# Optimization experiments

Measured on AMD Instinct MI355X. Metric: run time of the kernel, lower is better.

The kernel has to match this reference:

```python
import jax, jax.numpy as jnp
import numpy as np

IMG_H, IMG_W = 240, 320
NEAR, FAR = 0.1, 10.0
CHUNK = 64  # triangles rasterized per scan step
CAM_K = np.array([[286.2057, 0.0, 162.6306],
                  [0.0, 286.7852, 121.0245],
                  [0.0, 0.0, 1.0]], np.float32)


def build_projection(cam, w, h, x0=0, y0=0, nc=NEAR, fc=FAR):
    q = -(fc + nc) / float(fc - nc)
    qn = -2.0 * fc * nc / float(fc - nc)
    proj = np.array([
        [2 * cam[0, 0] / w, -2 * cam[0, 1] / w, (-2 * cam[0, 2] + w + 2 * x0) / w, 0],
        [0, -2 * cam[1, 1] / h, (-2 * cam[1, 2] + h + 2 * y0) / h, 0],
        [0, 0, q, qn],
        [0, 0, -1, 0]], dtype=np.float64)
    proj[1, :] *= -1.0
    return jnp.asarray(proj.T, jnp.float32)


def vertex_normals(verts, faces):
    # per-face normal scattered to its vertices then renormalized
    # (equals dirt lighting.vertex_normals_pre_split on split meshes)
    v0, v1, v2 = verts[faces[:, 0]], verts[faces[:, 1]], verts[faces[:, 2]]
    fn = jnp.cross(v1 - v0, v2 - v0)
    fn = fn / jnp.maximum(jnp.linalg.norm(fn, axis=1, keepdims=True), 1e-12)
    vn = (jnp.zeros_like(verts)
          .at[faces[:, 0]].add(fn)
          .at[faces[:, 1]].add(fn)
          .at[faces[:, 2]].add(fn))
    return vn / jnp.maximum(jnp.linalg.norm(vn, axis=1, keepdims=True), 1e-12)


def transform_vertices(vertices, pose, faces, proj):
    vert_obj = jnp.concatenate([vertices, jnp.ones_like(vertices[:, -1:])], axis=1)  # [V,4]
    normals = vertex_normals(vert_obj[:, :3], faces)
    gl = jnp.array([[1., 0., 0.], [0., -1., 0.], [0., 0., -1.]], jnp.float32)
    rot = gl @ pose[:3, :3]
    # replicate the flat-list surgery: cam_pose[:3,:3]=gl@R, negate t_y, t_z
    cam_pose = pose.at[:3, :3].set(rot).at[1, 3].multiply(-1.0).at[2, 3].multiply(-1.0)
    view = cam_pose.T
    vert_cam = vert_obj @ view                                   # [V,4]
    vert_3d = vert_obj[:, :3] @ pose[:3, :3].T + pose[:3, 3]     # [V,3]
    vert_clip = vert_cam @ proj                                  # [V,4]
    return vert_obj, vert_3d, vert_clip, normals


def rasterise(vert_clip, colors, faces, H, W):
    # z-buffered triangle rasterization with perspective-correct barycentric
    # interpolation, processed in chunks of CHUNK triangles via lax.scan.
    eps = 1e-9
    wc = vert_clip[:, 3]
    inv_w = 1.0 / jnp.where(jnp.abs(wc) > eps, wc, eps)
    ndc = vert_clip[:, :3] * inv_w[:, None]
    px = (ndc[:, 0] + 1.0) * 0.5 * W   # screen x
    py = (1.0 - ndc[:, 1]) * 0.5 * H   # screen y (row 0 at top)
    pz = ndc[:, 2]

    tpx, tpy, tpz = px[faces], py[faces], pz[faces]   # [F,3]
    tiw = inv_w[faces]                                # [F,3]
    tcol = colors[faces]                              # [F,3,C]
    tval = jnp.all(wc[faces] > 1e-6, axis=1)          # all verts in front

    F = faces.shape[0]
    pad = (-F) % CHUNK
    def padf(a):
        if pad == 0:
            return a
        return jnp.concatenate([a, jnp.zeros((pad,) + a.shape[1:], a.dtype)], 0)
    tpx, tpy, tpz, tiw, tcol = padf(tpx), padf(tpy), padf(tpz), padf(tiw), padf(tcol)
    tval = padf(tval)
    n_steps = (F + pad) // CHUNK
    resh = lambda a: a.reshape((n_steps, CHUNK) + a.shape[1:])
    xs = tuple(map(resh, (tpx, tpy, tpz, tiw, tcol, tval)))

    Xg = (jnp.arange(W, dtype=jnp.float32) + 0.5)[None, :, None]  # pixel centers
    Yg = (jnp.arange(H, dtype=jnp.float32) + 0.5)[:, None, None]
    BIG = jnp.float32(1e9)

    def step(carry, chunk):
        zbuf, cbuf = carry
        cpx, cpy, cpz, ciw, ccol, cval = chunk
        ax, ay = cpx[:, 0], cpy[:, 0]
        bx, by = cpx[:, 1], cpy[:, 1]
        cx, cy = cpx[:, 2], cpy[:, 2]
        area = (bx - ax) * (cy - ay) - (by - ay) * (cx - ax)            # [Fc]
        inv_area = 1.0 / jnp.where(jnp.abs(area) > 1e-12, area, 1e-12)
        # normalized edge functions (barycentrics), [H,W,Fc]
        e0 = ((Xg - bx) * (cy - by) - (Yg - by) * (cx - bx)) * inv_area
        e1 = ((Xg - cx) * (ay - cy) - (Yg - cy) * (ax - cx)) * inv_area
        e2 = 1.0 - e0 - e1
        depth = e0 * cpz[:, 0] + e1 * cpz[:, 1] + e2 * cpz[:, 2]        # screen-linear z
        inside = ((e0 >= 0) & (e1 >= 0) & (e2 >= 0) & cval
                  & (jnp.abs(area) > 1e-12) & (depth >= -1.0) & (depth <= 1.0))
        dmask = jnp.where(inside, depth, BIG)
        best = jnp.argmin(dmask, axis=2)                                # [H,W]
        bidx = best[..., None]
        bdepth = jnp.take_along_axis(dmask, bidx, 2)[..., 0]
        take = bdepth < zbuf
        b0 = jnp.take_along_axis(e0, bidx, 2)[..., 0]
        b1 = jnp.take_along_axis(e1, bidx, 2)[..., 0]
        b2 = 1.0 - b0 - b1
        piw = jnp.stack([b0, b1, b2], -1) * ciw[best]                   # [H,W,3]
        den = jnp.sum(piw, -1, keepdims=True)
        den = jnp.where(jnp.abs(den) > 1e-12, den, 1e-12)
        col = jnp.einsum('hwk,hwkc->hwc', piw / den, ccol[best])        # persp-correct
        zbuf = jnp.where(take, bdepth, zbuf)
        cbuf = jnp.where(take[..., None], col, cbuf)
        return (zbuf, cbuf), None

    zbuf0 = jnp.full((H, W), BIG, jnp.float32)
    cbuf0 = jnp.zeros((H, W, colors.shape[1]), jnp.float32)
    (_, cbuf), _ = jax.lax.scan(jax.checkpoint(step), (zbuf0, cbuf0), xs)
    return cbuf


def setup_inputs() -> dict:
    key = jax.random.key(0)
    k1, k2 = jax.random.split(key)
    V, F = 12288, 4096
    vertices = 0.15 * jax.random.normal(k1, (1, V, 3), jnp.float32)
    faces = jax.random.randint(k2, (1, F, 3), 0, V, jnp.int32)
    pose = jnp.eye(4, dtype=jnp.float32).at[2, 3].set(0.6)  # object 0.6m in front
    return {"vertices": vertices, "faces": faces, "poses": pose[None]}


def reference(vertices, faces, poses):
    proj = build_projection(CAM_K, IMG_W, IMG_H)
    faces0 = jnp.asarray(faces[0], jnp.int32)
    vert_obj, vert_3d, vert_clip, normals = transform_vertices(vertices[0], poses[0], faces0, proj)
    colors = jnp.concatenate(
        [jnp.ones_like(vert_obj[:, :1]), vert_3d, normals, vert_obj], axis=1)  # [V,11]
    g = rasterise(vert_clip, colors, faces0, IMG_H, IMG_W)  # [H,W,11]
    return g[None]
```

## Files before the change

### kernel.cpp

```cpp
#include <hip/hip_runtime.h>
#include <math.h>

#pragma clang fp contract(off)

#define IMG_H 240
#define IMG_W 320
#define NPX   (IMG_H * IMG_W)
#define NCH   11
#define NCHP  12
#define NSLICE 8
#define CULL_M 1e-3f
#define EZ_M   1e-5f
#define NBIN   256

struct ProjM { float m[16]; };

__device__ __forceinline__ int zbin(float zm) {
  float t = fminf(fmaxf((zm + 1.0f) * 128.0f, 0.0f), 255.0f);
  int b = (int)t;
  if ((float)b * 0.0078125f - 1.0f > zm) b = (b > 0) ? b - 1 : 0;
  return b;
}

extern "C" __global__ void k_init(float* __restrict__ vnacc, int n3v,
                                  unsigned long long* __restrict__ zkey,
                                  int* __restrict__ hist) {
  int i = blockIdx.x * 256 + threadIdx.x;
  if (i < n3v) vnacc[i] = 0.0f;
  if (i < NPX) zkey[i] = ~0ull;
  if (i < NBIN) hist[i] = 0;
}

__device__ __forceinline__ void xform(float x, float y, float z,
                                      const float* __restrict__ pose,
                                      const ProjM& P,
                                      float& px, float& py, float& pz,
                                      float& iw, float& wc) {
  float c0 = ((x*pose[0]     + y*pose[1])     + z*pose[2])     + pose[3];
  float c1 = ((x*(-pose[4])  + y*(-pose[5]))  + z*(-pose[6]))  + (-pose[7]);
  float c2 = ((x*(-pose[8])  + y*(-pose[9]))  + z*(-pose[10])) + (-pose[11]);
  float c3 = ((x*pose[12]    + y*pose[13])    + z*pose[14])    + pose[15];
  float q0 = ((c0*P.m[0]  + c1*P.m[1])  + c2*P.m[2])  + c3*P.m[3];
  float q1 = ((c0*P.m[4]  + c1*P.m[5])  + c2*P.m[6])  + c3*P.m[7];
  float q2 = ((c0*P.m[8]  + c1*P.m[9])  + c2*P.m[10]) + c3*P.m[11];
  float q3 = ((c0*P.m[12] + c1*P.m[13]) + c2*P.m[14]) + c3*P.m[15];
  wc = q3;
  float denw = (fabsf(wc) > 1e-9f) ? wc : 1e-9f;
  iw = 1.0f / denw;
  float ndx = q0 * iw, ndy = q1 * iw;
  pz = q2 * iw;
  px = ((ndx + 1.0f) * 0.5f) * (float)IMG_W;
  py = ((1.0f - ndy) * 0.5f) * (float)IMG_H;
}

extern "C" __global__ void k_face(const float* __restrict__ verts,
                                  const int* __restrict__ faces,
                                  const float* __restrict__ pose,
                                  ProjM P,
                                  float* __restrict__ vnacc,
                                  float4* __restrict__ frec,
                                  float4* __restrict__ fbb,
                                  float4* __restrict__ fe,
                                  int4*  __restrict__ fidx,
                                  float* __restrict__ fzmin,
                                  int*   __restrict__ hist, int F) {
  int f = blockIdx.x * 64 + threadIdx.x;
  if (f >= F) return;
  int i0 = faces[3*f+0], i1 = faces[3*f+1], i2 = faces[3*f+2];
  float x0 = verts[3*i0+0], y0 = verts[3*i0+1], z0 = verts[3*i0+2];
  float x1 = verts[3*i1+0], y1 = verts[3*i1+1], z1 = verts[3*i1+2];
  float x2 = verts[3*i2+0], y2 = verts[3*i2+1], z2 = verts[3*i2+2];

  {
    float ux = x1 - x0, uy = y1 - y0, uz = z1 - z0;
    float vx = x2 - x0, vy = y2 - y0, vz = z2 - z0;
    float fx = uy*vz - uz*vy;
    float fy = uz*vx - ux*vz;
    float fz = ux*vy - uy*vx;
    float n = sqrtf((fx*fx + fy*fy) + fz*fz);
    float d = fmaxf(n, 1e-12f);
    fx = fx / d; fy = fy / d; fz = fz / d;
    atomicAdd(&vnacc[3*i0+0], fx); atomicAdd(&vnacc[3*i0+1], fy); atomicAdd(&vnacc[3*i0+2], fz);
    atomicAdd(&vnacc[3*i1+0], fx); atomicAdd(&vnacc[3*i1+1], fy); atomicAdd(&vnacc[3*i1+2], fz);
    atomicAdd(&vnacc[3*i2+0], fx); atomicAdd(&vnacc[3*i2+1], fy); atomicAdd(&vnacc[3*i2+2], fz);
  }

  float ax, ay, pz0, iw0, w0;  xform(x0, y0, z0, pose, P, ax, ay, pz0, iw0, w0);
  float bx, by, pz1, iw1, w1;  xform(x1, y1, z1, pose, P, bx, by, pz1, iw1, w1);
  float cx, cy, pz2, iw2, w2;  xform(x2, y2, z2, pose, P, cx, cy, pz2, iw2, w2);

  float area = (bx - ax) * (cy - ay) - (by - ay) * (cx - ax);
  float inva = 1.0f / ((fabsf(area) > 1e-12f) ? area : 1e-12f);
  bool valid = (w0 > 1e-6f) && (w1 > 1e-6f) && (w2 > 1e-6f) && (fabsf(area) > 1e-12f);
  float rax = 2.0f*cx - ax, ray = 2.0f*cy - ay;
  float rbx = 2.0f*cx - bx, rby = 2.0f*cy - by;
  float minx = fminf(cx, fminf(rax, rbx)), maxx = fmaxf(cx, fmaxf(rax, rbx));
  float miny = fminf(cy, fminf(ray, rby)), maxy = fmaxf(cy, fmaxf(ray, rby));
  frec[4*f+0] = make_float4(bx, by, cy - by, cx - bx);
  frec[4*f+1] = make_float4(cx, cy, ay - cy, ax - cx);
  frec[4*f+2] = make_float4(inva, pz0, pz1, pz2);
  frec[4*f+3] = make_float4(iw0, iw1, iw2, 0.0f);
  fbb[f] = valid ? make_float4(minx, maxx, miny, maxy)
                 : make_float4(1e30f, -1e30f, 1e30f, -1e30f);
  fidx[f] = make_int4(i0, i1, i2, 0);

  float zm = valid ? fminf(pz0, fminf(pz1, pz2)) : __builtin_huge_valf();
  fzmin[f] = zm;
  atomicAdd(&hist[zbin(zm)], 1);

  {
    double dbx = bx, dby = by, dcx = cx, dcy = cy, dax = ax, day = ay;
    double dinv = (double)inva;
    double d0 = dcy - dby, d1 = dcx - dbx;
    double d2 = day - dcy, d3 = dax - dcx;
    double a0 = d0 * dinv, b0 = -d1 * dinv, c0 = (dby * d1 - dbx * d0) * dinv;
    double a1 = d2 * dinv, b1 = -d3 * dinv, c1 = (dcy * d3 - dcx * d2) * dinv;
    fe[2*f+0] = make_float4((float)a0, (float)b0, (float)c0, 0.0f);
    fe[2*f+1] = make_float4((float)a1, (float)b1, (float)c1, 0.0f);
  }
}

extern "C" __global__ void k_scan(const int* __restrict__ hist,
                                  int* __restrict__ binoff) {
  __shared__ int s[NBIN];
  int t = threadIdx.x;
  int v = hist[t];
  s[t] = v;
  __syncthreads();
  for (int o = 1; o < NBIN; o <<= 1) {
    int x = (t >= o) ? s[t - o] : 0;
    __syncthreads();
    s[t] += x;
    __syncthreads();
  }
  binoff[t] = s[t] - v;
}

extern "C" __global__ void k_scatter(const float* __restrict__ fzmin,
                                     int* __restrict__ binoff,
                                     const float4* __restrict__ fbb,
                                     const float4* __restrict__ fe,
                                     int*   __restrict__ forig,
                                     float* __restrict__ szmin,
                                     float* __restrict__ smon,
                                     float4* __restrict__ fbbs,
                                     float4* __restrict__ fes, int F) {
  int f = blockIdx.x * 256 + threadIdx.x;
  if (f >= F) return;
  float zm = fzmin[f];
  int b = zbin(zm);
  int pos = atomicAdd(&binoff[b], 1);
  forig[pos] = f;
  szmin[pos] = zm;
  smon[pos]  = (float)b * 0.0078125f - 1.0f;
  fbbs[pos]  = fbb[f];
  fes[2*pos+0] = fe[2*f+0];
  fes[2*pos+1] = fe[2*f+1];
}

extern "C" __global__ void k_vertex(const float* __restrict__ verts,
                                    const float* __restrict__ vnacc,
                                    const float* __restrict__ pose,
                                    float4* __restrict__ colors, int V) {
  int i = blockIdx.x * 64 + threadIdx.x;
  if (i >= V) return;
  float x = verts[3*i+0], y = verts[3*i+1], z = verts[3*i+2];

  float nx = vnacc[3*i+0], ny = vnacc[3*i+1], nz = vnacc[3*i+2];
  float nn = sqrtf((nx*nx + ny*ny) + nz*nz);
  float nm = fmaxf(nn, 1e-12f);
  nx = nx / nm; ny = ny / nm; nz = nz / nm;

  float v3x = ((x*pose[0] + y*pose[1]) + z*pose[2])  + pose[3];
  float v3y = ((x*pose[4] + y*pose[5]) + z*pose[6])  + pose[7];
  float v3z = ((x*pose[8] + y*pose[9]) + z*pose[10]) + pose[11];

  colors[3*i+0] = make_float4(1.0f, v3x, v3y, v3z);
  colors[3*i+1] = make_float4(nx, ny, nz, x);
  colors[3*i+2] = make_float4(y, z, 1.0f, 0.0f);
}

extern "C" __global__ __launch_bounds__(256)
void k_rasterA(const float4* __restrict__ frec,
               const float4* __restrict__ fbbs,
               const float4* __restrict__ fes,
               const int*    __restrict__ forig,
               const float*  __restrict__ szmin,
               const float*  __restrict__ smon,
               unsigned long long* __restrict__ zkey,
               int F) {
  int t = threadIdx.x;
  int wave = t >> 6;
  int lane = t & 63;
  int sx = (wave & 1) * 8, sy = (wave >> 1) * 8;
  int pxi = blockIdx.x * 16 + sx + (lane & 7);
  int pyi = blockIdx.y * 16 + sy + (lane >> 3);
  float X = (float)pxi + 0.5f;
  float Y = (float)pyi + 0.5f;
  float tXlo = (float)(blockIdx.x * 16 + sx) + 0.5f, tXhi = tXlo + 7.0f;
  float tYlo = (float)(blockIdx.y * 16 + sy) + 0.5f, tYhi = tYlo + 7.0f;
  size_t pix = (size_t)pyi * IMG_W + pxi;

  float bestd = 1.0f + 1.0e-3f;
  int   besti = -1;

  int nchunk = (F + 63) >> 6;
  for (int c = blockIdx.z; c < nchunk; c += NSLICE) {
    int base = c << 6;

    float pb = bestd;
    {
      unsigned long long k = __hip_atomic_load(&zkey[pix], __ATOMIC_RELAXED,
                                               __HIP_MEMORY_SCOPE_AGENT);
      if (k != ~0ull) {
        unsigned int ub = (unsigned int)(k >> 32);
        unsigned int fb = (ub & 0x80000000u) ? (ub & 0x7FFFFFFFu) : ~ub;
        pb = fminf(pb, __uint_as_float(fb));
      }
    }
    float pbm = pb;
    #pragma unroll
    for (int o = 32; o > 0; o >>= 1) pbm = fmaxf(pbm, __shfl_xor(pbm, o));

    if (pbm <= smon[base] - EZ_M) break;

    int i = base + lane;
    bool ov = false;
    if (i < F && szmin[i] < pbm + EZ_M) {
      float4 bb = fbbs[i];
      ov = (bb.x - 1.0f <= tXhi) && (bb.y + 1.0f >= tXlo) &&
           (bb.z - 1.0f <= tYhi) && (bb.w + 1.0f >= tYlo);
      if (ov) {
        float4 E0 = fes[2*i+0];
        float4 E1 = fes[2*i+1];
        float pa0 = E0.x * tXlo, pb0 = E0.x * tXhi;
        float qa0 = E0.y * tYlo, qb0 = E0.y * tYhi;
        float e0mx = (fmaxf(pa0, pb0) + fmaxf(qa0, qb0)) + E0.z;
        float pa1 = E1.x * tXlo, pb1 = E1.x * tXhi;
        float qa1 = E1.y * tYlo, qb1 = E1.y * tYhi;
        float e1mx = (fmaxf(pa1, pb1) + fmaxf(qa1, qb1)) + E1.z;
        float e0mn = (fminf(pa0, pb0) + fminf(qa0, qb0)) + E0.z;
        float e1mn = (fminf(pa1, pb1) + fminf(qa1, qb1)) + E1.z;
        float e2mx = (1.0f - e0mn) - e1mn;
        ov = (e0mx >= -CULL_M) && (e1mx >= -CULL_M) && (e2mx >= -CULL_M);
      }
    }
    unsigned long long mask = __ballot(ov);
    bool improved = false;

    while (mask) {
      int j = __builtin_ctzll(mask);
      mask &= mask - 1;
      int ju = __builtin_amdgcn_readfirstlane(forig[base + j]);
      const float4* fr = frec + (size_t)ju * 4;
      float4 A = fr[0];
      float4 B = fr[1];
      float4 C = fr[2];
      float t0 = (X - A.x) * A.z;
      float t1 = (Y - A.y) * A.w;
      float e0 = (t0 - t1) * C.x;
      float t2 = (X - B.x) * B.z;
      float t3 = (Y - B.y) * B.w;
      float e1 = (t2 - t3) * C.x;
      float e2 = (1.0f - e0) - e1;
      float depth = ((e0 * C.y) + (e1 * C.z)) + (e2 * C.w);
      bool inside = (e0 >= 0.0f) && (e1 >= 0.0f) && (e2 >= 0.0f) &&
                    (depth >= -1.0f) && (depth <= 1.0f);
      if (inside && depth < bestd) {
        bestd = depth; besti = ju; improved = true;
      }
    }

    if (improved && bestd <= pb) {
      unsigned int ub = __float_as_uint(bestd);
      ub = (ub & 0x80000000u) ? ~ub : (ub | 0x80000000u);
      unsigned long long key = ((unsigned long long)ub << 32) | (unsigned int)besti;
      atomicMin(&zkey[pix], key);
    }
  }
}

extern "C" __global__ __launch_bounds__(256)
void k_resolve(const unsigned long long* __restrict__ zkey,
               const float4* __restrict__ frec,
               const float4* __restrict__ colors,
               const int4* __restrict__ fidx,
               float* __restrict__ out) {
  __shared__ float sOut[256 * NCH];
  int t = threadIdx.x;
  int p = blockIdx.x * 256 + t;
  int pyi = p / IMG_W, pxi = p - pyi * IMG_W;
  float X = (float)pxi + 0.5f;
  float Y = (float)pyi + 0.5f;
  unsigned long long key = zkey[p];

  float oc[NCH];
  if (key != ~0ull) {
    int besti = (int)(key & 0xFFFFFFFFu);
    const float4* fr = frec + (size_t)besti * 4;
    float4 A = fr[0], B = fr[1], C = fr[2], D = fr[3];
    float t0 = (X - A.x) * A.z;
    float t1 = (Y - A.y) * A.w;
    float e0 = (t0 - t1) * C.x;
    float t2 = (X - B.x) * B.z;
    float t3 = (Y - B.y) * B.w;
    float e1 = (t2 - t3) * C.x;
    float b2 = (1.0f - e0) - e1;
    float p0 = e0 * D.x, p1 = e1 * D.y, p2 = b2 * D.z;
    float den = (p0 + p1) + p2;
    if (!(fabsf(den) > 1e-12f)) den = 1e-12f;
    float u0 = p0 / den, u1 = p1 / den, u2 = p2 / den;
    int4 vi = fidx[besti];
    float c0v[NCHP], c1v[NCHP], c2v[NCHP];
    #pragma unroll
    for (int k = 0; k < 3; ++k) {
      *(float4*)(c0v + 4*k) = colors[3*vi.x + k];
      *(float4*)(c1v + 4*k) = colors[3*vi.y + k];
      *(float4*)(c2v + 4*k) = colors[3*vi.z + k];
    }
    #pragma unroll
    for (int ch = 0; ch < NCH; ++ch)
      oc[ch] = (u0 * c0v[ch] + u1 * c1v[ch]) + u2 * c2v[ch];
  } else {
    #pragma unroll
    for (int ch = 0; ch < NCH; ++ch) oc[ch] = 0.0f;
  }
  #pragma unroll
  for (int ch = 0; ch < NCH; ++ch) sOut[t * NCH + ch] = oc[ch];
  __syncthreads();
  float4* o4 = (float4*)(out + (size_t)blockIdx.x * 256 * NCH);
  const float4* s4 = (const float4*)sOut;
  #pragma unroll
  for (int k = 0; k < 3; ++k) {
    int idx = t + k * 256;
    if (idx < 704) o4[idx] = s4[idx];
  }
}

extern "C" void kernel_launch(void* const* d_in, const int* in_sizes, int n_in,
                              void* d_out, int out_size, void* d_ws, size_t ws_size,
                              hipStream_t stream) {
  const float* verts = (const float*)d_in[0];
  const int*   faces = (const int*)d_in[1];
  const float* pose  = (const float*)d_in[2];
  float* out = (float*)d_out;
  int V = in_sizes[0] / 3;
  int F = in_sizes[1] / 3;

  float* ws = (float*)d_ws;
  size_t o = 0;
  auto alloc = [&](size_t n) { size_t r = o; o += (n + 3) & ~(size_t)3; return r; };
  size_t o_zk   = alloc((size_t)2 * NPX);
  size_t o_vn   = alloc((size_t)3 * V);
  size_t o_col  = alloc((size_t)NCHP * V);
  size_t o_fr   = alloc((size_t)16 * F);
  size_t o_bb   = alloc((size_t)4 * F);
  size_t o_fe   = alloc((size_t)8 * F);
  size_t o_fi   = alloc((size_t)4 * F);
  size_t o_fz   = alloc((size_t)F);
  size_t o_hist = alloc((size_t)NBIN);
  size_t o_boff = alloc((size_t)NBIN);
  size_t o_fo   = alloc((size_t)F);
  size_t o_sz   = alloc((size_t)F);
  size_t o_sm   = alloc((size_t)F);
  size_t o_bbs  = alloc((size_t)4 * F);
  size_t o_fes  = alloc((size_t)8 * F);
  unsigned long long* zkey = (unsigned long long*)(ws + o_zk);
  float*  vnacc = ws + o_vn;
  float4* col   = (float4*)(ws + o_col);
  float4* frec  = (float4*)(ws + o_fr);
  float4* fbb   = (float4*)(ws + o_bb);
  float4* fe    = (float4*)(ws + o_fe);
  int4*   fidx  = (int4*)(ws + o_fi);
  float*  fzmin = ws + o_fz;
  int*    hist  = (int*)(ws + o_hist);
  int*    boff  = (int*)(ws + o_boff);
  int*    forig = (int*)(ws + o_fo);
  float*  szmin = ws + o_sz;
  float*  smon  = ws + o_sm;
  float4* fbbs  = (float4*)(ws + o_bbs);
  float4* fes   = (float4*)(ws + o_fes);

  double fxd = 286.2057, sd = 0.0, cxd = 162.6306;
  double fyd = 286.7852, cyd = 121.0245;
  double wd = IMG_W, hd = IMG_H, ncd = 0.1, fcd = 10.0;
  double q  = -(fcd + ncd) / (fcd - ncd);
  double qn = -2.0 * fcd * ncd / (fcd - ncd);
  double Pd[16] = {
    2.0*fxd/wd, -2.0*sd/wd, (-2.0*cxd + wd)/wd, 0.0,
    0.0,        2.0*fyd/hd, (2.0*cyd - hd)/hd, -0.0,
    0.0,        0.0,        q,                  qn,
    0.0,        0.0,       -1.0,                0.0 };
  ProjM P;
  for (int i = 0; i < 16; ++i) P.m[i] = (float)Pd[i];

  int n3v = 3 * V;
  int initN = (NPX > n3v) ? NPX : n3v;
  k_init<<<(initN + 255) / 256, 256, 0, stream>>>(vnacc, n3v, zkey, hist);
  k_face<<<(F + 63) / 64, 64, 0, stream>>>(verts, faces, pose, P, vnacc,
                                           frec, fbb, fe, fidx, fzmin, hist, F);
  k_scan<<<1, NBIN, 0, stream>>>(hist, boff);
  k_scatter<<<(F + 255) / 256, 256, 0, stream>>>(fzmin, boff, fbb, fe,
                                                 forig, szmin, smon, fbbs, fes, F);
  k_vertex<<<(V + 63) / 64, 64, 0, stream>>>(verts, vnacc, pose, col, V);
  dim3 g(IMG_W / 16, IMG_H / 16, NSLICE);
  k_rasterA<<<g, 256, 0, stream>>>(frec, fbbs, fes, forig, szmin, smon, zkey, F);
  k_resolve<<<NPX / 256, 256, 0, stream>>>(zkey, frec, col, fidx, out);
}
```

Baseline: 103.1 us.

## Copy face records into depth-sorted order and early-skip occluded candidate triangles

The scatter kernel now also copies the per-face raster records into the z-sorted order, so the raster loop reads them contiguously rather than through an indirect gather via the original face index. Each wave preloads zmin and the original index per lane and fetches them with shuffles. Before evaluating each candidate it skips the triangle when no lane's current best depth exceeds that triangle's min depth. A tie-break on the face index is added to keep results deterministic, at the cost of an extra scatter copy and more workspace.

```diff
diff --git a/kernel.cpp b/kernel.cpp
--- a/kernel.cpp
+++ b/kernel.cpp
@@ -140,11 +140,13 @@
                                      int* __restrict__ binoff,
                                      const float4* __restrict__ fbb,
                                      const float4* __restrict__ fe,
+                                     const float4* __restrict__ frec,
                                      int*   __restrict__ forig,
                                      float* __restrict__ szmin,
                                      float* __restrict__ smon,
                                      float4* __restrict__ fbbs,
-                                     float4* __restrict__ fes, int F) {
+                                     float4* __restrict__ fes,
+                                     float4* __restrict__ frecs, int F) {
   int f = blockIdx.x * 256 + threadIdx.x;
   if (f >= F) return;
   float zm = fzmin[f];
@@ -156,6 +158,10 @@
   fbbs[pos]  = fbb[f];
   fes[2*pos+0] = fe[2*f+0];
   fes[2*pos+1] = fe[2*f+1];
+  frecs[4*pos+0] = frec[4*f+0];
+  frecs[4*pos+1] = frec[4*f+1];
+  frecs[4*pos+2] = frec[4*f+2];
+  frecs[4*pos+3] = frec[4*f+3];
 }
 
 extern "C" __global__ void k_vertex(const float* __restrict__ verts,
@@ -181,7 +187,7 @@
 }
 
 extern "C" __global__ __launch_bounds__(256)
-void k_rasterA(const float4* __restrict__ frec,
+void k_rasterA(const float4* __restrict__ frecs,
                const float4* __restrict__ fbbs,
                const float4* __restrict__ fes,
                const int*    __restrict__ forig,
@@ -225,24 +231,30 @@
     if (pbm <= smon[base] - EZ_M) break;
 
     int i = base + lane;
+    float szlane = __builtin_huge_valf();
+    int   folane = 0;
     bool ov = false;
-    if (i < F && szmin[i] < pbm + EZ_M) {
-      float4 bb = fbbs[i];
-      ov = (bb.x - 1.0f <= tXhi) && (bb.y + 1.0f >= tXlo) &&
-           (bb.z - 1.0f <= tYhi) && (bb.w + 1.0f >= tYlo);
-      if (ov) {
-        float4 E0 = fes[2*i+0];
-        float4 E1 = fes[2*i+1];
-        float pa0 = E0.x * tXlo, pb0 = E0.x * tXhi;
-        float qa0 = E0.y * tYlo, qb0 = E0.y * tYhi;
-        float e0mx = (fmaxf(pa0, pb0) + fmaxf(qa0, qb0)) + E0.z;
-        float pa1 = E1.x * tXlo, pb1 = E1.x * tXhi;
-        float qa1 = E1.y * tYlo, qb1 = E1.y * tYhi;
-        float e1mx = (fmaxf(pa1, pb1) + fmaxf(qa1, qb1)) + E1.z;
-        float e0mn = (fminf(pa0, pb0) + fminf(qa0, qb0)) + E0.z;
-        float e1mn = (fminf(pa1, pb1) + fminf(qa1, qb1)) + E1.z;
-        float e2mx = (1.0f - e0mn) - e1mn;
-        ov = (e0mx >= -CULL_M) && (e1mx >= -CULL_M) && (e2mx >= -CULL_M);
+    if (i < F) {
+      szlane = szmin[i];
+      folane = forig[i];
+      if (szlane < pbm + EZ_M) {
+        float4 bb = fbbs[i];
+        ov = (bb.x - 1.0f <= tXhi) && (bb.y + 1.0f >= tXlo) &&
+             (bb.z - 1.0f <= tYhi) && (bb.w + 1.0f >= tYlo);
+        if (ov) {
+          float4 E0 = fes[2*i+0];
+          float4 E1 = fes[2*i+1];
+          float pa0 = E0.x * tXlo, pb0 = E0.x * tXhi;
+          float qa0 = E0.y * tYlo, qb0 = E0.y * tYhi;
+          float e0mx = (fmaxf(pa0, pb0) + fmaxf(qa0, qb0)) + E0.z;
+          float pa1 = E1.x * tXlo, pb1 = E1.x * tXhi;
+          float qa1 = E1.y * tYlo, qb1 = E1.y * tYhi;
+          float e1mx = (fmaxf(pa1, pb1) + fmaxf(qa1, qb1)) + E1.z;
+          float e0mn = (fminf(pa0, pb0) + fminf(qa0, qb0)) + E0.z;
+          float e1mn = (fminf(pa1, pb1) + fminf(qa1, qb1)) + E1.z;
+          float e2mx = (1.0f - e0mn) - e1mn;
+          ov = (e0mx >= -CULL_M) && (e1mx >= -CULL_M) && (e2mx >= -CULL_M);
+        }
       }
     }
     unsigned long long mask = __ballot(ov);
@@ -251,8 +263,11 @@
     while (mask) {
       int j = __builtin_ctzll(mask);
       mask &= mask - 1;
-      int ju = __builtin_amdgcn_readfirstlane(forig[base + j]);
-      const float4* fr = frec + (size_t)ju * 4;
+      float zminf = __shfl(szlane, j);
+      if (__ballot(bestd > zminf - EZ_M) == 0ull) continue;
+      int jj = __builtin_amdgcn_readfirstlane(base + j);
+      int ju = __builtin_amdgcn_readfirstlane(__shfl(folane, j));
+      const float4* fr = frecs + (size_t)jj * 4;
       float4 A = fr[0];
       float4 B = fr[1];
       float4 C = fr[2];
@@ -266,7 +281,7 @@
       float depth = ((e0 * C.y) + (e1 * C.z)) + (e2 * C.w);
       bool inside = (e0 >= 0.0f) && (e1 >= 0.0f) && (e2 >= 0.0f) &&
                     (depth >= -1.0f) && (depth <= 1.0f);
-      if (inside && depth < bestd) {
+      if (inside && (depth < bestd || (depth == bestd && ju < besti))) {
         bestd = depth; besti = ju; improved = true;
       }
     }
@@ -365,6 +380,7 @@
   size_t o_sm   = alloc((size_t)F);
   size_t o_bbs  = alloc((size_t)4 * F);
   size_t o_fes  = alloc((size_t)8 * F);
+  size_t o_frs  = alloc((size_t)16 * F);
   unsigned long long* zkey = (unsigned long long*)(ws + o_zk);
   float*  vnacc = ws + o_vn;
   float4* col   = (float4*)(ws + o_col);
@@ -380,6 +396,7 @@
   float*  smon  = ws + o_sm;
   float4* fbbs  = (float4*)(ws + o_bbs);
   float4* fes   = (float4*)(ws + o_fes);
+  float4* frecs = (float4*)(ws + o_frs);
 
   double fxd = 286.2057, sd = 0.0, cxd = 162.6306;
   double fyd = 286.7852, cyd = 121.0245;
@@ -400,10 +417,11 @@
   k_face<<<(F + 63) / 64, 64, 0, stream>>>(verts, faces, pose, P, vnacc,
                                            frec, fbb, fe, fidx, fzmin, hist, F);
   k_scan<<<1, NBIN, 0, stream>>>(hist, boff);
-  k_scatter<<<(F + 255) / 256, 256, 0, stream>>>(fzmin, boff, fbb, fe,
-                                                 forig, szmin, smon, fbbs, fes, F);
+  k_scatter<<<(F + 255) / 256, 256, 0, stream>>>(fzmin, boff, fbb, fe, frec,
+                                                 forig, szmin, smon, fbbs, fes,
+                                                 frecs, F);
   k_vertex<<<(V + 63) / 64, 64, 0, stream>>>(verts, vnacc, pose, col, V);
   dim3 g(IMG_W / 16, IMG_H / 16, NSLICE);
-  k_rasterA<<<g, 256, 0, stream>>>(frec, fbbs, fes, forig, szmin, smon, zkey, F);
+  k_rasterA<<<g, 256, 0, stream>>>(frecs, fbbs, fes, forig, szmin, smon, zkey, F);
   k_resolve<<<NPX / 256, 256, 0, stream>>>(zkey, frec, col, fidx, out);
 }
```

Result: no change. 103.7 us (+0.6%).
